# Kernel optimization log

Hardware: AMD Instinct MI355X
Metric: run time of the kernel (lower is better)

The kernel has to match this reference:

```python
import jax, jax.numpy as jnp
import numpy as np

B, H, W, C = 16, 64, 64, 256
WS = 8          # window_size
SHIFT = 4       # shift_size
HEADS = 8
HEAD_DIM = C // HEADS
N = WS * WS     # tokens per window
HID = 4 * C     # mlp hidden
EPS = 1e-5


def _rel_pos_index():
    coords = np.stack(np.meshgrid(np.arange(WS), np.arange(WS), indexing='ij'))  # [2,WS,WS]
    flat = coords.reshape(2, -1)                                                  # [2,N]
    rel = (flat[:, :, None] - flat[:, None, :]).transpose(1, 2, 0)                # [N,N,2]
    rel[:, :, 0] += WS - 1
    rel[:, :, 1] += WS - 1
    rel[:, :, 0] *= 2 * WS - 1
    return rel.sum(-1).astype(np.int32)                                           # [N,N]


def _attn_mask():
    # shifted-window region ids, identical to get_img_mask (shift == WS//2)
    img = np.zeros((H, W), dtype=np.float32)
    cnt = 0
    for hs in (slice(0, H - WS), slice(H - WS, H - SHIFT), slice(H - SHIFT, H)):
        for ws_ in (slice(0, W - WS), slice(W - WS, W - SHIFT), slice(W - SHIFT, W)):
            img[hs, ws_] = cnt
            cnt += 1
    mw = img.reshape(H // WS, WS, W // WS, WS).transpose(0, 2, 1, 3).reshape(-1, N)  # [nW,N]
    diff = mw[:, None, :] - mw[:, :, None]
    return np.where(diff != 0, -100.0, 0.0).astype(np.float32)                        # [nW,N,N]


def window_partition(x):
    # [B,H,W,C] -> [B*nW, N, C]
    x = x.reshape(B, H // WS, WS, W // WS, WS, C)
    return x.transpose(0, 1, 3, 2, 4, 5).reshape(-1, N, C)


def window_reverse(w):
    # [B*nW, WS, WS, C] -> [B,H,W,C]
    x = w.reshape(B, H // WS, W // WS, WS, WS, C)
    return x.transpose(0, 1, 3, 2, 4, 5).reshape(B, H, W, C)


def layernorm(x, g, b):
    mu = jnp.mean(x, -1, keepdims=True)
    var = jnp.mean(jnp.square(x - mu), -1, keepdims=True)
    return (x - mu) * jax.lax.rsqrt(var + EPS) * g + b


def setup_inputs() -> dict:
    key = jax.random.key(0)
    ks = jax.random.split(key, 12)
    s = 0.02
    return {
        'x': jax.random.normal(ks[0], (B, H, W, C), jnp.float32),
        'ln1_g': jnp.ones((C,), jnp.float32),
        'ln1_b': jnp.zeros((C,), jnp.float32),
        'qkv_w': jax.random.normal(ks[1], (C, 3 * C), jnp.float32) * s,
        'qkv_b': jnp.zeros((3 * C,), jnp.float32),
        'proj_w': jax.random.normal(ks[2], (C, C), jnp.float32) * s,
        'proj_b': jnp.zeros((C,), jnp.float32),
        'rel_bias_table': jax.random.normal(ks[3], ((2 * WS - 1) ** 2, HEADS), jnp.float32) * s,
        'ln2_g': jnp.ones((C,), jnp.float32),
        'ln2_b': jnp.zeros((C,), jnp.float32),
        'mlp_w1': jax.random.normal(ks[4], (C, HID), jnp.float32) * s,
        'mlp_b1': jnp.zeros((HID,), jnp.float32),
        'mlp_w2': jax.random.normal(ks[5], (HID, C), jnp.float32) * s,
        'mlp_b2': jnp.zeros((C,), jnp.float32),
        'rel_index': jnp.asarray(_rel_pos_index()),  # [N,N] int32, constant
    }


def reference(x, ln1_g, ln1_b, qkv_w, qkv_b, proj_w, proj_b, rel_bias_table,
              ln2_g, ln2_b, mlp_w1, mlp_b1, mlp_w2, mlp_b2, rel_index):
    attn_mask = jnp.asarray(_attn_mask())                 # [nW,N,N]
    nW = attn_mask.shape[0]

    shortcut = x.reshape(B, H * W, C)
    h = layernorm(shortcut, ln1_g, ln1_b).reshape(B, H, W, C)

    # cyclic shift + window partition
    h = jnp.roll(h, shift=(-SHIFT, -SHIFT), axis=(1, 2))
    xw = window_partition(h)                              # [B*nW, N, C]

    # window attention with relative position bias
    qkv = xw @ qkv_w + qkv_b                              # [B*nW, N, 3C]
    qkv = qkv.reshape(-1, N, 3, HEADS, HEAD_DIM).transpose(2, 0, 3, 1, 4)
    q, k, v = qkv[0], qkv[1], qkv[2]                      # [B*nW, heads, N, hd]
    attn = jnp.einsum('whnd,whmd->whnm', q * (HEAD_DIM ** -0.5), k)
    bias = rel_bias_table[rel_index]                      # [N,N,heads]
    attn = attn + bias.transpose(2, 0, 1)[None]           # [B*nW,heads,N,N]
    attn = attn.reshape(B, nW, HEADS, N, N) + attn_mask[None, :, None]
    attn = jax.nn.softmax(attn.reshape(-1, HEADS, N, N), axis=-1)
    out = jnp.einsum('whnm,whmd->whnd', attn, v)
    out = out.transpose(0, 2, 1, 3).reshape(-1, N, C)
    out = out @ proj_w + proj_b                           # [B*nW, N, C]

    # window reverse + reverse shift
    out = window_reverse(out.reshape(-1, WS, WS, C))
    out = jnp.roll(out, shift=(SHIFT, SHIFT), axis=(1, 2)).reshape(B, H * W, C)

    h = shortcut + out
    m = layernorm(h, ln2_g, ln2_b)
    m = jax.nn.gelu(m @ mlp_w1 + mlp_b1) @ mlp_w2 + mlp_b2
    h = h + m
    return h.reshape(B, H, W, C)
```

## Files before the change

kernel.cpp:

```cpp
#include <hip/hip_runtime.h>


typedef __attribute__((ext_vector_type(8))) short bf16x8;
typedef __attribute__((ext_vector_type(4))) float f32x4;
typedef __attribute__((ext_vector_type(16))) float f32x16;

__device__ __forceinline__ float bf2f(unsigned short h) {
    union { unsigned int u; float f; } c; c.u = ((unsigned int)h) << 16; return c.f;
}
__device__ __forceinline__ unsigned short f2bf(float f) {
    union { float f; unsigned int u; } c; c.f = f;
    unsigned int u = c.u;
    return (unsigned short)((u + 0x7FFFu + ((u >> 16) & 1u)) >> 16);
}
__device__ __forceinline__ unsigned int cvtpk_bf16(float lo, float hi) {
    unsigned int r;
    asm volatile("v_cvt_pk_bf16_f32 %0, %1, %2" : "=v"(r) : "v"(lo), "v"(hi));
    return r;
}
__device__ __forceinline__ void perm32swap(unsigned int& a, unsigned int& b) {
    asm volatile("v_permlane32_swap_b32 %0, %1" : "+v"(a), "+v"(b));
}
__device__ __forceinline__ int remap_row(int row) {
    int b  = row >> 12;
    int w6 = (row >> 6) & 63;
    int n  = row & 63;
    int hp = (((w6 >> 3) << 3) + (n >> 3) + 4) & 63;
    int wp = (((w6 & 7) << 3) + (n & 7) + 4) & 63;
    return (b << 12) | (hp << 6) | wp;
}
__device__ __forceinline__ float gelu_f(float v) {
    float u = 1.5957691216057308f * (v + 0.044715f * v * v * v);
    return v / (1.0f + __expf(-u));
}
__device__ __forceinline__ void gload16(const unsigned short* g, unsigned short* l) {
    __builtin_amdgcn_global_load_lds(
        (const __attribute__((address_space(1))) void*)g,
        (__attribute__((address_space(3))) void*)l, 16, 0, 0);
}

template<int INBF>
__global__ __launch_bounds__(256) void ln_kernel(
    const void* __restrict__ inp, const float* __restrict__ g,
    const float* __restrict__ b, unsigned short* __restrict__ out, int remap)
{
    int wave = threadIdx.x >> 6, lane = threadIdx.x & 63;
    int row = (blockIdx.x << 2) + wave;
    int src = remap ? remap_row(row) : row;
    float4 xv;
    if (INBF) {
        ushort4 u = *(const ushort4*)((const unsigned short*)inp + (size_t)src * 256 + (lane << 2));
        xv.x = bf2f(u.x); xv.y = bf2f(u.y); xv.z = bf2f(u.z); xv.w = bf2f(u.w);
    } else {
        xv = *(const float4*)((const float*)inp + (size_t)src * 256 + (lane << 2));
    }
    float s  = xv.x + xv.y + xv.z + xv.w;
    float ss = xv.x*xv.x + xv.y*xv.y + xv.z*xv.z + xv.w*xv.w;
#pragma unroll
    for (int off = 32; off; off >>= 1) {
        s  += __shfl_xor(s,  off, 64);
        ss += __shfl_xor(ss, off, 64);
    }
    float mu  = s * (1.0f / 256.0f);
    float inv = rsqrtf(ss * (1.0f / 256.0f) - mu * mu + 1e-5f);
    float4 gv = *(const float4*)(g + (lane << 2));
    float4 bv = *(const float4*)(b + (lane << 2));
    ushort4 o;
    o.x = f2bf((xv.x - mu) * inv * gv.x + bv.x);
    o.y = f2bf((xv.y - mu) * inv * gv.y + bv.y);
    o.z = f2bf((xv.z - mu) * inv * gv.z + bv.z);
    o.w = f2bf((xv.w - mu) * inv * gv.w + bv.w);
    *(ushort4*)(out + (size_t)row * 256 + (lane << 2)) = o;
}

__device__ __forceinline__ void convT_body(
    const float* __restrict__ in, unsigned short* __restrict__ out,
    int K, int N, int b, float (*t)[33], int tid)
{
    int kb = K >> 5;
    int bk = (b % kb) << 5;
    int bn = (b / kb) << 5;
    int r = tid >> 5, c = tid & 31;
#pragma unroll
    for (int i = 0; i < 4; ++i)
        t[r + i * 8][c] = in[(size_t)(bk + r + i * 8) * N + bn + c];
    __syncthreads();
#pragma unroll
    for (int i = 0; i < 4; ++i)
        out[(size_t)(bn + r + i * 8) * K + bk + c] = f2bf(t[c][r + i * 8]);
}

__global__ __launch_bounds__(256) void prep_kernel(
    const float* __restrict__ qkv_w, const float* __restrict__ proj_w,
    const float* __restrict__ w1, const float* __restrict__ w2,
    unsigned short* __restrict__ qkvT, unsigned short* __restrict__ prjT,
    unsigned short* __restrict__ w1T, unsigned short* __restrict__ w2T,
    const float* __restrict__ table, const int* __restrict__ relidx,
    float* __restrict__ bexp)
{
    __shared__ float t[32][33];
    const int b = blockIdx.x, tid = threadIdx.x;
    if      (b < 192) convT_body(qkv_w, qkvT, 256,  768, b,       t, tid);
    else if (b < 256) convT_body(proj_w, prjT, 256,  256, b - 192, t, tid);
    else if (b < 512) convT_body(w1,    w1T,  256, 1024, b - 256, t, tid);
    else if (b < 768) convT_body(w2,    w2T, 1024,  256, b - 512, t, tid);
    else {
        int i = (b - 768) * 256 + tid;
        int head = i >> 12;
        int q = (i >> 6) & 63;
        int k = i & 63;
        bexp[i] = table[relidx[q * 64 + k] * 8 + head];
    }
}

template<int OUT_BF16, int DO_GELU, int RESID, int QSCALE, int RESBF>
__global__ __launch_bounds__(512, 2) void mgemm_kernel(
    const unsigned short* __restrict__ A, const unsigned short* __restrict__ BT,
    const float* __restrict__ bias, void* __restrict__ outp,
    const void* __restrict__ resid, int M, int N, int K)
{
    __shared__ __align__(16) unsigned short smem[32768];
#define ASB(b) (smem + (b) * 4096)
#define BSB(b) (smem + 16384 + (b) * 4096)

    const int cpx = (int)gridDim.x >> 3;
    const int bid = ((int)blockIdx.x & 7) * cpx + ((int)blockIdx.x >> 3);

    const int nb = N >> 7;
    const int m0 = (bid / nb) << 7;
    const int n0 = (bid % nb) << 7;
    const int tid  = threadIdx.x;
    const int wid  = tid >> 6;
    const int lane = tid & 63;
    const int wm = (wid >> 1) << 5;
    const int wn = (wid & 1) << 6;

    const unsigned short* Ag = A  + (size_t)m0 * K;
    const unsigned short* Bg = BT + (size_t)n0 * K;
    const size_t ra = (size_t)(tid >> 2) * K + (((tid & 3) ^ ((tid >> 2) & 3)) << 3);

    f32x4 acc[4][2] = {};
    const int fr = lane & 15;
    const int fq = lane >> 4;
    const int axor = ((fq ^ (fr & 3)) << 3);

#define STAGE(buf, kk)                                                        \
    {                                                                         \
        gload16(Ag + ra + (kk), ASB(buf) + tid * 8);                          \
        gload16(Bg + ra + (kk), BSB(buf) + tid * 8);                          \
    }

    const int NIT = K >> 5;
    STAGE(0, 0);
    STAGE(1, 32);
    STAGE(2, 64);

    for (int t = 0; t < NIT; ++t) {
        if (t + 2 < NIT)      asm volatile("s_waitcnt vmcnt(4)" ::: "memory");
        else if (t + 1 < NIT) asm volatile("s_waitcnt vmcnt(2)" ::: "memory");
        else                  asm volatile("s_waitcnt vmcnt(0)" ::: "memory");
        __builtin_amdgcn_s_barrier();

        const int cur = t & 3;
        bf16x8 af[2], bfr[4];
#pragma unroll
        for (int i = 0; i < 2; ++i)
            af[i] = *(const bf16x8*)(ASB(cur) + (wm + i * 16 + fr) * 32 + axor);
#pragma unroll
        for (int j = 0; j < 4; ++j)
            bfr[j] = *(const bf16x8*)(BSB(cur) + (wn + j * 16 + fr) * 32 + axor);
#pragma unroll
        for (int j = 0; j < 4; ++j)
#pragma unroll
            for (int i = 0; i < 2; ++i)
                acc[j][i] = __builtin_amdgcn_mfma_f32_16x16x32_bf16(
                    bfr[j], af[i], acc[j][i], 0, 0, 0);

        if (t + 3 < NIT) STAGE((t + 3) & 3, (t + 3) << 5);
    }
#undef STAGE

    __builtin_amdgcn_s_barrier();

#pragma unroll
    for (int j = 0; j < 4; ++j) {
        const int fc = wn + j * 16 + (fq << 2);
        const int gcol = n0 + fc;
        const float4 b4 = *(const float4*)(bias + gcol);
#pragma unroll
        for (int i = 0; i < 2; ++i) {
            const int row = wm + i * 16 + fr;
            float v0 = acc[j][i][0] + b4.x;
            float v1 = acc[j][i][1] + b4.y;
            float v2 = acc[j][i][2] + b4.z;
            float v3 = acc[j][i][3] + b4.w;
            if (QSCALE && gcol < 256) {
                v0 *= 0.17677669529663687f; v1 *= 0.17677669529663687f;
                v2 *= 0.17677669529663687f; v3 *= 0.17677669529663687f;
            }
            if (DO_GELU) {
                v0 = gelu_f(v0); v1 = gelu_f(v1); v2 = gelu_f(v2); v3 = gelu_f(v3);
            }
            if (OUT_BF16) {
                uint2 pp;
                pp.x = cvtpk_bf16(v0, v1);
                pp.y = cvtpk_bf16(v2, v3);
                const int u = (row << 5) + ((fc >> 2) ^ (row & 6));
                *(uint2*)((char*)smem + (size_t)u * 8) = pp;
            } else {
                float4 o4; o4.x = v0; o4.y = v1; o4.z = v2; o4.w = v3;
                const int u = (row << 5) + ((fc >> 2) ^ (row & 7));
                *(float4*)((char*)smem + (size_t)u * 16) = o4;
            }
        }
    }
    __builtin_amdgcn_s_barrier();

    if (OUT_BF16) {
#pragma unroll
        for (int p = 0; p < 4; ++p) {
            const int row = (p << 5) + (tid >> 4);
            const int q = tid & 15;
            const int u = (row << 5) + ((q << 1) ^ (row & 6));
            uint4 a = *(const uint4*)((const char*)smem + (size_t)u * 8);
            const int grow = m0 + row;
            const int orow = (RESID == 2) ? remap_row(grow) : grow;
            const int gcol = n0 + (q << 3);
            if (RESID) {
                float rv[8];
                if (RESBF) {
                    ushort4 ra_ = *(const ushort4*)((const unsigned short*)resid
                                                    + (size_t)orow * N + gcol);
                    ushort4 rb_ = *(const ushort4*)((const unsigned short*)resid
                                                    + (size_t)orow * N + gcol + 4);
                    rv[0]=bf2f(ra_.x); rv[1]=bf2f(ra_.y); rv[2]=bf2f(ra_.z); rv[3]=bf2f(ra_.w);
                    rv[4]=bf2f(rb_.x); rv[5]=bf2f(rb_.y); rv[6]=bf2f(rb_.z); rv[7]=bf2f(rb_.w);
                } else {
                    float4 ra_ = *(const float4*)((const float*)resid + (size_t)orow * N + gcol);
                    float4 rb_ = *(const float4*)((const float*)resid + (size_t)orow * N + gcol + 4);
                    rv[0]=ra_.x; rv[1]=ra_.y; rv[2]=ra_.z; rv[3]=ra_.w;
                    rv[4]=rb_.x; rv[5]=rb_.y; rv[6]=rb_.z; rv[7]=rb_.w;
                }
                const unsigned short* s = (const unsigned short*)&a;
                uint4 o;
                o.x = cvtpk_bf16(bf2f(s[0]) + rv[0], bf2f(s[1]) + rv[1]);
                o.y = cvtpk_bf16(bf2f(s[2]) + rv[2], bf2f(s[3]) + rv[3]);
                o.z = cvtpk_bf16(bf2f(s[4]) + rv[4], bf2f(s[5]) + rv[5]);
                o.w = cvtpk_bf16(bf2f(s[6]) + rv[6], bf2f(s[7]) + rv[7]);
                a = o;
            }
            *(uint4*)((unsigned short*)outp + (size_t)orow * N + gcol) = a;
        }
    } else {
#pragma unroll
        for (int p = 0; p < 8; ++p) {
            const int row = (p << 4) + (tid >> 5);
            const int q = tid & 31;
            const int u = (row << 5) + (q ^ (row & 7));
            float4 v = *(const float4*)((const char*)smem + (size_t)u * 16);
            const int grow = m0 + row;
            const int orow = (RESID == 2) ? remap_row(grow) : grow;
            const int gcol = n0 + (q << 2);
            if (RESID) {
                if (RESBF) {
                    ushort4 r4 = *(const ushort4*)((const unsigned short*)resid
                                                   + (size_t)orow * N + gcol);
                    v.x += bf2f(r4.x); v.y += bf2f(r4.y);
                    v.z += bf2f(r4.z); v.w += bf2f(r4.w);
                } else {
                    float4 r4 = *(const float4*)((const float*)resid + (size_t)orow * N + gcol);
                    v.x += r4.x; v.y += r4.y; v.z += r4.z; v.w += r4.w;
                }
            }
            *(float4*)((float*)outp + (size_t)orow * N + gcol) = v;
        }
    }
#undef ASB
#undef BSB
}

__global__ __launch_bounds__(64, 3) void attn_kernel(
    const unsigned short* __restrict__ qkv,
    const float* __restrict__ bexp,
    unsigned short* __restrict__ out)
{
    __shared__ unsigned short VT[2048];
    const int bid  = blockIdx.x;
    const int widx = bid & 1023;
    const int head = bid >> 10;
    const int l  = threadIdx.x;
    const int lo = l & 31, hi = l >> 5;

    const unsigned short* base = qkv + (size_t)widx * 64 * 768;

#pragma unroll
    for (int c = 0; c < 4; ++c) {
        union { bf16x8 v; unsigned short s[8]; } u;
        u.v = *(const bf16x8*)(base + (size_t)l * 768 + 512 + head * 32 + c * 8);
#pragma unroll
        for (int e = 0; e < 8; ++e) {
            int d = c * 8 + e;
            int wb = ((d * 64 + l) * 2) ^ ((d & 7) << 4);
            *(unsigned short*)((char*)VT + wb) = u.s[e];
        }
    }

    f32x16 acc[2][2] = {};
#pragma unroll
    for (int kd = 0; kd < 2; ++kd) {
        const int coff = head * 32 + kd * 16 + hi * 8;
        bf16x8 kf0 = *(const bf16x8*)(base + (size_t)lo        * 768 + 256 + coff);
        bf16x8 kf1 = *(const bf16x8*)(base + (size_t)(32 + lo) * 768 + 256 + coff);
        bf16x8 qf0 = *(const bf16x8*)(base + (size_t)lo        * 768 + coff);
        bf16x8 qf1 = *(const bf16x8*)(base + (size_t)(32 + lo) * 768 + coff);
        acc[0][0] = __builtin_amdgcn_mfma_f32_32x32x16_bf16(kf0, qf0, acc[0][0], 0, 0, 0);
        acc[0][1] = __builtin_amdgcn_mfma_f32_32x32x16_bf16(kf0, qf1, acc[0][1], 0, 0, 0);
        acc[1][0] = __builtin_amdgcn_mfma_f32_32x32x16_bf16(kf1, qf0, acc[1][0], 0, 0, 0);
        acc[1][1] = __builtin_amdgcn_mfma_f32_32x32x16_bf16(kf1, qf1, acc[1][1], 0, 0, 0);
    }

#pragma unroll
    for (int qb = 0; qb < 2; ++qb) {
        const float* bq = bexp + head * 4096 + (qb * 32 + lo) * 64;
#pragma unroll
        for (int kb = 0; kb < 2; ++kb)
#pragma unroll
            for (int j = 0; j < 4; ++j) {
                float4 b4 = *(const float4*)(bq + kb * 32 + j * 8 + hi * 4);
                acc[kb][qb][4 * j + 0] += b4.x;
                acc[kb][qb][4 * j + 1] += b4.y;
                acc[kb][qb][4 * j + 2] += b4.z;
                acc[kb][qb][4 * j + 3] += b4.w;
            }
    }

    const int w6 = widx & 63;
    if (((w6 >> 3) == 7) || ((w6 & 7) == 7)) {
#pragma unroll
        for (int qb = 0; qb < 2; ++qb) {
            int nq = qb * 32 + lo;
            int phq = ((w6 >> 3) << 3) + (nq >> 3), pwq = ((w6 & 7) << 3) + (nq & 7);
            int rq = ((phq < 56) ? 0 : ((phq < 60) ? 1 : 2)) * 3
                   + ((pwq < 56) ? 0 : ((pwq < 60) ? 1 : 2));
#pragma unroll
            for (int kb = 0; kb < 2; ++kb)
#pragma unroll
                for (int r = 0; r < 16; ++r) {
                    int nk = kb * 32 + (r & 3) + 8 * (r >> 2) + 4 * hi;
                    int phk = ((w6 >> 3) << 3) + (nk >> 3), pwk = ((w6 & 7) << 3) + (nk & 7);
                    int rk = ((phk < 56) ? 0 : ((phk < 60) ? 1 : 2)) * 3
                           + ((pwk < 56) ? 0 : ((pwk < 60) ? 1 : 2));
                    if (rk != rq) acc[kb][qb][r] -= 100.0f;
                }
        }
    }

#pragma unroll
    for (int qb = 0; qb < 2; ++qb) {
        float mx = acc[0][qb][0];
#pragma unroll
        for (int r = 1; r < 16; ++r) mx = fmaxf(mx, acc[0][qb][r]);
#pragma unroll
        for (int r = 0; r < 16; ++r) mx = fmaxf(mx, acc[1][qb][r]);
        mx = fmaxf(mx, __shfl_xor(mx, 32, 64));
        float sum = 0.f;
#pragma unroll
        for (int kb = 0; kb < 2; ++kb)
#pragma unroll
            for (int r = 0; r < 16; ++r) {
                float e = __expf(acc[kb][qb][r] - mx);
                acc[kb][qb][r] = e;
                sum += e;
            }
        sum += __shfl_xor(sum, 32, 64);
        float inv = 1.0f / sum;
#pragma unroll
        for (int kb = 0; kb < 2; ++kb)
#pragma unroll
            for (int r = 0; r < 16; ++r) acc[kb][qb][r] *= inv;
    }

    f32x16 o[2] = {};
#pragma unroll
    for (int ks = 0; ks < 4; ++ks) {
        const int s8 = (ks & 1) * 8, kb = ks >> 1;
        const int rb = ((lo * 64 + 16 * ks + 8 * hi) * 2) ^ ((lo & 7) << 4);
        bf16x8 vb = *(const bf16x8*)((const char*)VT + rb);
#pragma unroll
        for (int qb = 0; qb < 2; ++qb) {
            unsigned int a0 = cvtpk_bf16(acc[kb][qb][s8 + 0], acc[kb][qb][s8 + 1]);
            unsigned int b0 = cvtpk_bf16(acc[kb][qb][s8 + 4], acc[kb][qb][s8 + 5]);
            unsigned int a1 = cvtpk_bf16(acc[kb][qb][s8 + 2], acc[kb][qb][s8 + 3]);
            unsigned int b1 = cvtpk_bf16(acc[kb][qb][s8 + 6], acc[kb][qb][s8 + 7]);
            perm32swap(a0, b0);
            perm32swap(a1, b1);
            union { unsigned int u[4]; bf16x8 v; } w;
            w.u[0] = a0; w.u[1] = a1; w.u[2] = b0; w.u[3] = b1;
            o[qb] = __builtin_amdgcn_mfma_f32_32x32x16_bf16(w.v, vb, o[qb], 0, 0, 0);
        }
    }

    unsigned short* ob = out + (size_t)widx * 64 * 256 + head * 32 + lo;
#pragma unroll
    for (int qb = 0; qb < 2; ++qb)
#pragma unroll
        for (int r = 0; r < 16; ++r) {
            int q = qb * 32 + (r & 3) + 8 * (r >> 2) + 4 * hi;
            ob[(size_t)q * 256] = f2bf(o[qb][r]);
        }
}

extern "C" void kernel_launch(void* const* d_in, const int* in_sizes, int n_in,
                              void* d_out, int out_size, void* d_ws, size_t ws_size,
                              hipStream_t stream)
{
    const float* x      = (const float*)d_in[0];
    const float* ln1_g  = (const float*)d_in[1];
    const float* ln1_b  = (const float*)d_in[2];
    const float* qkv_w  = (const float*)d_in[3];
    const float* qkv_b  = (const float*)d_in[4];
    const float* proj_w = (const float*)d_in[5];
    const float* proj_b = (const float*)d_in[6];
    const float* table  = (const float*)d_in[7];
    const float* ln2_g  = (const float*)d_in[8];
    const float* ln2_b  = (const float*)d_in[9];
    const float* w1     = (const float*)d_in[10];
    const float* b1     = (const float*)d_in[11];
    const float* w2     = (const float*)d_in[12];
    const float* b2     = (const float*)d_in[13];
    const int*   relidx = (const int*)d_in[14];
    float* out = (float*)d_out;

    char* w = (char*)d_ws;
    unsigned short* xw   = (unsigned short*)w;
    unsigned short* qkvb = (unsigned short*)(w + (32u << 20));
    unsigned short* h2b  = (unsigned short*)(w + (160u << 20));
    float*          bexp = (float*)(w + (224u << 20));
    unsigned short* qkvT = (unsigned short*)(w + (224u << 20) + (128u << 10));
    unsigned short* prjT = qkvT + 768 * 256;
    unsigned short* w1T  = prjT + 256 * 256;
    unsigned short* w2T  = w1T + 1024 * 256;

    prep_kernel<<<896, 256, 0, stream>>>(qkv_w, proj_w, w1, w2,
                                         qkvT, prjT, w1T, w2T,
                                         table, relidx, bexp);
    ln_kernel<0><<<16384, 256, 0, stream>>>(x, ln1_g, ln1_b, xw, 1);
    mgemm_kernel<1, 0, 0, 1, 0><<<512 * 6, 512, 0, stream>>>(
        xw, qkvT, qkv_b, (void*)qkvb, nullptr, 65536, 768, 256);
    attn_kernel<<<8192, 64, 0, stream>>>(qkvb, bexp, xw);
    mgemm_kernel<1, 0, 2, 0, 0><<<512 * 2, 512, 0, stream>>>(
        xw, prjT, proj_b, (void*)h2b, x, 65536, 256, 256);
    ln_kernel<1><<<16384, 256, 0, stream>>>(h2b, ln2_g, ln2_b, xw, 0);
    mgemm_kernel<1, 1, 0, 0, 0><<<512 * 8, 512, 0, stream>>>(
        xw, w1T, b1, (void*)qkvb, nullptr, 65536, 1024, 256);
    mgemm_kernel<0, 0, 1, 0, 1><<<512 * 2, 512, 0, stream>>>(
        qkvb, w2T, b2, (void*)out, h2b, 65536, 256, 1024);
}
```

Baseline: 292.5 us.

## Fuse QKV projection into window attention kernel, one block per window

Replaces the separate QKV GEMM and per-head attention kernel with a single kernel where each 512-thread block loads one window's normalized tokens into shared memory once. Each wave computes its head's Q, K and V slices with MFMA and keeps them in registers as operands, folding in the scale and bias. Output is staged through shared memory for coalesced stores. This removes the round trip of the 65536x768 QKV intermediate through global memory. In exchange, each block reads its weights straight from global memory without cross-block reuse, and register pressure is higher.

```diff
diff --git a/kernel.cpp b/kernel.cpp
--- a/kernel.cpp
+++ b/kernel.cpp
@@ -279,44 +279,98 @@
 #undef BSB
 }
 
-__global__ __launch_bounds__(64, 3) void attn_kernel(
-    const unsigned short* __restrict__ qkv,
+__global__ __launch_bounds__(512, 2) void qkvattn_kernel(
+    const unsigned short* __restrict__ xw,
+    const unsigned short* __restrict__ qkvT,
+    const float* __restrict__ qkv_b,
     const float* __restrict__ bexp,
     unsigned short* __restrict__ out)
 {
-    __shared__ unsigned short VT[2048];
-    const int bid  = blockIdx.x;
-    const int widx = bid & 1023;
-    const int head = bid >> 10;
-    const int l  = threadIdx.x;
-    const int lo = l & 31, hi = l >> 5;
-
-    const unsigned short* base = qkv + (size_t)widx * 64 * 768;
-
-#pragma unroll
-    for (int c = 0; c < 4; ++c) {
-        union { bf16x8 v; unsigned short s[8]; } u;
-        u.v = *(const bf16x8*)(base + (size_t)l * 768 + 512 + head * 32 + c * 8);
-#pragma unroll
-        for (int e = 0; e < 8; ++e) {
-            int d = c * 8 + e;
-            int wb = ((d * 64 + l) * 2) ^ ((d & 7) << 4);
-            *(unsigned short*)((char*)VT + wb) = u.s[e];
+    __shared__ __align__(16) unsigned short Asm[16384];
+    const int widx = blockIdx.x;
+    const int tid  = threadIdx.x;
+    const int head = tid >> 6;
+    const int l    = tid & 63;
+    const int lo   = l & 31, hi = l >> 5;
+
+    {
+        const unsigned short* Ag = xw + ((size_t)widx << 6) * 256;
+#pragma unroll
+        for (int i = 0; i < 4; ++i) {
+            int u = tid + (i << 9);
+            int r = u >> 5, p = u & 31;
+            int lg = (p & 24) | ((p ^ r) & 7);
+            gload16(Ag + (size_t)r * 256 + lg * 8, Asm + u * 8);
+        }
+        asm volatile("s_waitcnt vmcnt(0)" ::: "memory");
+        __builtin_amdgcn_s_barrier();
+    }
+
+#define AREAD(tok, kk)                                                         \
+    (*(const bf16x8*)(Asm + (tok) * 256 +                                      \
+        (((((kk) >> 3) + hi) & 24) | (((((kk) >> 3) + hi) ^ (tok)) & 7)) * 8))
+
+#define DANCE(aa, op0, op1)                                                    \
+    {                                                                          \
+        _Pragma("unroll")                                                      \
+        for (int kd_ = 0; kd_ < 2; ++kd_) {                                    \
+            const int s8_ = kd_ * 8;                                           \
+            unsigned int a0 = cvtpk_bf16((aa)[s8_ + 0], (aa)[s8_ + 1]);        \
+            unsigned int b0 = cvtpk_bf16((aa)[s8_ + 4], (aa)[s8_ + 5]);        \
+            unsigned int a1 = cvtpk_bf16((aa)[s8_ + 2], (aa)[s8_ + 3]);        \
+            unsigned int b1 = cvtpk_bf16((aa)[s8_ + 6], (aa)[s8_ + 7]);        \
+            perm32swap(a0, b0);                                                \
+            perm32swap(a1, b1);                                                \
+            union { unsigned int u[4]; bf16x8 v; } w_;                         \
+            w_.u[0] = a0; w_.u[1] = a1; w_.u[2] = b0; w_.u[3] = b1;            \
+            if (kd_) (op1) = w_.v; else (op0) = w_.v;                          \
+        }                                                                      \
+    }
+
+    bf16x8 opK[2][2], opQ[2][2];
+
+#pragma unroll
+    for (int mat = 0; mat < 2; ++mat) {
+        const int sec = mat ? 0 : 1;
+        const unsigned short* Wb = qkvT + ((size_t)(sec * 256 + head * 32 + lo)) * 256 + 8 * hi;
+        f32x16 ac[2] = {};
+#pragma unroll
+        for (int kk = 0; kk < 256; kk += 16) {
+            bf16x8 wf = *(const bf16x8*)(Wb + kk);
+#pragma unroll
+            for (int tb = 0; tb < 2; ++tb)
+                ac[tb] = __builtin_amdgcn_mfma_f32_32x32x16_bf16(
+                    wf, AREAD(lo + 32 * tb, kk), ac[tb], 0, 0, 0);
+        }
+        const float* bb = qkv_b + sec * 256 + head * 32 + 4 * hi;
+#pragma unroll
+        for (int tb = 0; tb < 2; ++tb) {
+#pragma unroll
+            for (int qd = 0; qd < 4; ++qd) {
+                float4 b4 = *(const float4*)(bb + 8 * qd);
+                ac[tb][4 * qd + 0] += b4.x;
+                ac[tb][4 * qd + 1] += b4.y;
+                ac[tb][4 * qd + 2] += b4.z;
+                ac[tb][4 * qd + 3] += b4.w;
+                if (sec == 0) {
+                    ac[tb][4 * qd + 0] *= 0.17677669529663687f;
+                    ac[tb][4 * qd + 1] *= 0.17677669529663687f;
+                    ac[tb][4 * qd + 2] *= 0.17677669529663687f;
+                    ac[tb][4 * qd + 3] *= 0.17677669529663687f;
+                }
+            }
+            if (sec == 1) { DANCE(ac[tb], opK[tb][0], opK[tb][1]); }
+            else          { DANCE(ac[tb], opQ[tb][0], opQ[tb][1]); }
         }
     }
 
     f32x16 acc[2][2] = {};
 #pragma unroll
     for (int kd = 0; kd < 2; ++kd) {
-        const int coff = head * 32 + kd * 16 + hi * 8;
-        bf16x8 kf0 = *(const bf16x8*)(base + (size_t)lo        * 768 + 256 + coff);
-        bf16x8 kf1 = *(const bf16x8*)(base + (size_t)(32 + lo) * 768 + 256 + coff);
-        bf16x8 qf0 = *(const bf16x8*)(base + (size_t)lo        * 768 + coff);
-        bf16x8 qf1 = *(const bf16x8*)(base + (size_t)(32 + lo) * 768 + coff);
-        acc[0][0] = __builtin_amdgcn_mfma_f32_32x32x16_bf16(kf0, qf0, acc[0][0], 0, 0, 0);
-        acc[0][1] = __builtin_amdgcn_mfma_f32_32x32x16_bf16(kf0, qf1, acc[0][1], 0, 0, 0);
-        acc[1][0] = __builtin_amdgcn_mfma_f32_32x32x16_bf16(kf1, qf0, acc[1][0], 0, 0, 0);
-        acc[1][1] = __builtin_amdgcn_mfma_f32_32x32x16_bf16(kf1, qf1, acc[1][1], 0, 0, 0);
+        acc[0][0] = __builtin_amdgcn_mfma_f32_32x32x16_bf16(opK[0][kd], opQ[0][kd], acc[0][0], 0, 0, 0);
+        acc[0][1] = __builtin_amdgcn_mfma_f32_32x32x16_bf16(opK[0][kd], opQ[1][kd], acc[0][1], 0, 0, 0);
+        acc[1][0] = __builtin_amdgcn_mfma_f32_32x32x16_bf16(opK[1][kd], opQ[0][kd], acc[1][0], 0, 0, 0);
+        acc[1][1] = __builtin_amdgcn_mfma_f32_32x32x16_bf16(opK[1][kd], opQ[1][kd], acc[1][1], 0, 0, 0);
     }
 
 #pragma unroll
@@ -380,12 +434,32 @@
             for (int r = 0; r < 16; ++r) acc[kb][qb][r] *= inv;
     }
 
+    bf16x8 vop[2][2];
+    {
+        const unsigned short* Wb = qkvT + ((size_t)(512 + head * 32 + lo)) * 256 + 8 * hi;
+        f32x16 av[2] = {};
+#pragma unroll
+        for (int kk = 0; kk < 256; kk += 16) {
+            bf16x8 wf = *(const bf16x8*)(Wb + kk);
+#pragma unroll
+            for (int tb = 0; tb < 2; ++tb)
+                av[tb] = __builtin_amdgcn_mfma_f32_32x32x16_bf16(
+                    AREAD(lo + 32 * tb, kk), wf, av[tb], 0, 0, 0);
+        }
+        const float bv = qkv_b[512 + head * 32 + lo];
+#pragma unroll
+        for (int tb = 0; tb < 2; ++tb) {
+#pragma unroll
+            for (int r = 0; r < 16; ++r) av[tb][r] += bv;
+            DANCE(av[tb], vop[tb][0], vop[tb][1]);
+        }
+    }
+
     f32x16 o[2] = {};
 #pragma unroll
     for (int ks = 0; ks < 4; ++ks) {
         const int s8 = (ks & 1) * 8, kb = ks >> 1;
-        const int rb = ((lo * 64 + 16 * ks + 8 * hi) * 2) ^ ((lo & 7) << 4);
-        bf16x8 vb = *(const bf16x8*)((const char*)VT + rb);
+        bf16x8 vb = vop[ks >> 1][ks & 1];
 #pragma unroll
         for (int qb = 0; qb < 2; ++qb) {
             unsigned int a0 = cvtpk_bf16(acc[kb][qb][s8 + 0], acc[kb][qb][s8 + 1]);
@@ -400,14 +474,26 @@
         }
     }
 
-    unsigned short* ob = out + (size_t)widx * 64 * 256 + head * 32 + lo;
+    __builtin_amdgcn_s_barrier();
 #pragma unroll
     for (int qb = 0; qb < 2; ++qb)
 #pragma unroll
         for (int r = 0; r < 16; ++r) {
             int q = qb * 32 + (r & 3) + 8 * (r >> 2) + 4 * hi;
-            ob[(size_t)q * 256] = f2bf(o[qb][r]);
-        }
+            *(unsigned short*)((char*)Asm + q * 512 + head * 64 + lo * 2) = f2bf(o[qb][r]);
+        }
+    __builtin_amdgcn_s_barrier();
+    {
+        unsigned short* ob = out + ((size_t)widx << 6) * 256;
+#pragma unroll
+        for (int i = 0; i < 4; ++i) {
+            int u = tid + (i << 9);
+            uint4 vv = *(const uint4*)((const char*)Asm + (size_t)u * 16);
+            *(uint4*)(ob + (size_t)(u >> 5) * 256 + (u & 31) * 8) = vv;
+        }
+    }
+#undef AREAD
+#undef DANCE
 }
 
 extern "C" void kernel_launch(void* const* d_in, const int* in_sizes, int n_in,
@@ -445,11 +531,9 @@
                                          qkvT, prjT, w1T, w2T,
                                          table, relidx, bexp);
     ln_kernel<0><<<16384, 256, 0, stream>>>(x, ln1_g, ln1_b, xw, 1);
-    mgemm_kernel<1, 0, 0, 1, 0><<<512 * 6, 512, 0, stream>>>(
-        xw, qkvT, qkv_b, (void*)qkvb, nullptr, 65536, 768, 256);
-    attn_kernel<<<8192, 64, 0, stream>>>(qkvb, bexp, xw);
+    qkvattn_kernel<<<1024, 512, 0, stream>>>(xw, qkvT, qkv_b, bexp, qkvb);
     mgemm_kernel<1, 0, 2, 0, 0><<<512 * 2, 512, 0, stream>>>(
-        xw, prjT, proj_b, (void*)h2b, x, 65536, 256, 256);
+        qkvb, prjT, proj_b, (void*)h2b, x, 65536, 256, 256);
     ln_kernel<1><<<16384, 256, 0, stream>>>(h2b, ln2_g, ln2_b, xw, 0);
     mgemm_kernel<1, 1, 0, 0, 0><<<512 * 8, 512, 0, stream>>>(
         xw, w1T, b1, (void*)qkvb, nullptr, 65536, 1024, 256);
```

After: 282.7 us. 3.3% less time.
